# Kernel optimization log

Measured on AMD Instinct MI355X. Metric: run time of the kernel, lower is better.

## Reference

```python
import jax, jax.numpy as jnp
import numpy as np

N_FEAT = 128
F_HID = 128


def setup_inputs() -> dict:
    key = jax.random.key(0)
    ks = jax.random.split(key, 9)
    N, E = 100000, 1600000
    x = jax.random.normal(ks[0], (N, N_FEAT), dtype=jnp.float32)
    edge_index = jax.random.randint(ks[1], (2, E), 0, N, dtype=jnp.int64)
    def glorot(k, fan_in, fan_out):
        lim = np.sqrt(6.0 / (fan_in + fan_out)).astype(np.float32)
        return jax.random.uniform(k, (fan_in, fan_out), jnp.float32, -lim, lim)
    return {
        "x": x,
        "edge_index": edge_index,
        "W1": glorot(ks[2], N_FEAT, F_HID), "b1": jnp.zeros((F_HID,), jnp.float32),
        "W2": glorot(ks[3], F_HID, F_HID), "b2": jnp.zeros((F_HID,), jnp.float32),
        "W3": glorot(ks[4], F_HID, F_HID), "b3": jnp.zeros((F_HID,), jnp.float32),
    }


def _gcn_conv(x, W, b, row, col, inv_sqrt_deg, n):
    # GCNConv: x' = D^{-1/2} (A + I) D^{-1/2} (x @ W) + b  (self-loops already in row/col)
    h = x @ W                                   # [N, F]
    norm = inv_sqrt_deg[row] * inv_sqrt_deg[col]  # [E']
    msg = h[col] * norm[:, None]                # gather + scale, [E', F]
    out = jax.ops.segment_sum(msg, row, num_segments=n)  # scatter-add, [N, F]
    return out + b


def reference(x, edge_index, W1, b1, W2, b2, W3, b3):
    n = x.shape[0]
    loops = jnp.arange(n, dtype=edge_index.dtype)
    row = jnp.concatenate([edge_index[0], loops])
    col = jnp.concatenate([edge_index[1], loops])
    deg = jax.ops.segment_sum(jnp.ones_like(row, dtype=x.dtype), row, num_segments=n)
    inv_sqrt_deg = jnp.where(deg > 0, jax.lax.rsqrt(jnp.maximum(deg, 1.0)), 0.0)
    h = _gcn_conv(x, W1, b1, row, col, inv_sqrt_deg, n)
    h = jax.nn.relu(h)  # dropout is identity in eval mode
    h = _gcn_conv(h, W2, b2, row, col, inv_sqrt_deg, n)
    h = jax.nn.relu(h)
    h = _gcn_conv(h, W3, b3, row, col, inv_sqrt_deg, n)
    return h
```

## Files before the change

kernel.cpp:

```cpp
#include <hip/hip_runtime.h>
#include <hip/hip_bf16.h>

#define NFEAT 128
#define EPB   4096
#define RPB   256
#define NBU_PAD 512
#define BCAP  6144

typedef short bf16x8 __attribute__((ext_vector_type(8)));
typedef float f32x4  __attribute__((ext_vector_type(4)));

__global__ __launch_bounds__(256) void a1_hist(const int* __restrict__ rows, int E,
                                               int* __restrict__ countsT, int nbu) {
    __shared__ int h[NBU_PAD];
    int t = threadIdx.x;
    for (int i = t; i < NBU_PAD; i += 256) h[i] = 0;
    __syncthreads();
    int e0 = blockIdx.x * EPB;
    int ecnt = min(EPB, E - e0);
    for (int k = t; k < ecnt; k += 256) atomicAdd(&h[rows[e0 + k] >> 8], 1);
    __syncthreads();
    for (int j = t; j < nbu; j += 256) countsT[(size_t)blockIdx.x * nbu + j] = h[j];
}

__global__ void transpose_counts(const int* __restrict__ in, int* __restrict__ out,
                                 int nbk, int nbu) {
    int i = blockIdx.x * 256 + threadIdx.x;
    if (i < nbk * nbu) {
        int b = i / nbk, blk = i - b * nbk;
        out[i] = in[(size_t)blk * nbu + b];
    }
}

#define SCAN_B 1024
__global__ void scanA_kernel(const int* __restrict__ in, int K,
                             int* __restrict__ excl, int* __restrict__ bsums) {
    __shared__ int sm[SCAN_B];
    int t = threadIdx.x;
    int g = blockIdx.x * SCAN_B + t;
    int v = (g < K) ? in[g] : 0;
    sm[t] = v;
    __syncthreads();
    for (int off = 1; off < SCAN_B; off <<= 1) {
        int u = (t >= off) ? sm[t - off] : 0;
        __syncthreads();
        sm[t] += u;
        __syncthreads();
    }
    if (g < K) excl[g] = sm[t] - v;
    if (t == SCAN_B - 1) bsums[blockIdx.x] = sm[t];
}

__global__ void scanB_kernel(int* __restrict__ bsums, int nb) {
    __shared__ int s[256];
    int t = threadIdx.x;
    int v = (t < nb) ? bsums[t] : 0;
    s[t] = v;
    __syncthreads();
    for (int off = 1; off < 256; off <<= 1) {
        int u = (t >= off) ? s[t - off] : 0;
        __syncthreads();
        s[t] += u;
        __syncthreads();
    }
    if (t < nb) bsums[t] = s[t] - v;
}

__global__ void scanC_kernel(int* __restrict__ excl, const int* __restrict__ bsums, int K) {
    int g = blockIdx.x * 256 + threadIdx.x;
    if (g < K) excl[g] += bsums[g >> 10];
}

__global__ __launch_bounds__(256) void a2_scatter(const int* __restrict__ rows,
                                                  const int* __restrict__ colsIn, int E,
                                                  const int* __restrict__ scanArr,
                                                  int nbk, int nbu,
                                                  int* __restrict__ packed) {
    __shared__ int cnt[NBU_PAD], start[NBU_PAD], cur[NBU_PAD];
    __shared__ int sortedV[EPB];
    __shared__ unsigned short sortedB[EPB];
    __shared__ int p[256];
    int t = threadIdx.x, blk = blockIdx.x;
    for (int i = t; i < NBU_PAD; i += 256) cnt[i] = 0;
    __syncthreads();
    int e0 = blk * EPB;
    int ecnt = min(EPB, E - e0);
    int myr[16], myc[16];
#pragma unroll
    for (int k = 0; k < 16; ++k) {
        int idx = k * 256 + t;
        if (idx < ecnt) {
            myr[k] = rows[e0 + idx];
            myc[k] = colsIn[e0 + idx];
            atomicAdd(&cnt[myr[k] >> 8], 1);
        }
    }
    __syncthreads();
    int a0 = cnt[2 * t], a1 = cnt[2 * t + 1];
    p[t] = a0 + a1;
    __syncthreads();
    for (int off = 1; off < 256; off <<= 1) {
        int u = (t >= off) ? p[t - off] : 0;
        __syncthreads();
        p[t] += u;
        __syncthreads();
    }
    int ex = p[t] - (a0 + a1);
    start[2 * t] = ex;      start[2 * t + 1] = ex + a0;
    cur[2 * t] = ex;        cur[2 * t + 1] = ex + a0;
    __syncthreads();
#pragma unroll
    for (int k = 0; k < 16; ++k) {
        int idx = k * 256 + t;
        if (idx < ecnt) {
            int b = myr[k] >> 8;
            int pos = atomicAdd(&cur[b], 1);
            sortedV[pos] = ((myr[k] & 255) << 17) | myc[k];
            sortedB[pos] = (unsigned short)b;
        }
    }
    __syncthreads();
    for (int j = t; j < nbu; j += 256) cnt[j] = scanArr[(size_t)j * nbk + blk] - start[j];
    __syncthreads();
    for (int i = t; i < ecnt; i += 256) {
        int b = sortedB[i];
        packed[cnt[b] + i] = sortedV[i];
    }
}

__global__ __launch_bounds__(256) void b_sort(const int* __restrict__ packed,
                                              const int* __restrict__ scanArr,
                                              int nbk, int nbu, int N, int E,
                                              int* __restrict__ colSort,
                                              int* __restrict__ row_ptr,
                                              float* __restrict__ inv) {
    __shared__ int cnt[RPB], start[RPB], cur[RPB], s[RPB];
    __shared__ int sv[BCAP];
    int t = threadIdx.x, b = blockIdx.x;
    int base = scanArr[(size_t)b * nbk];
    int nxt = (b + 1 < nbu) ? scanArr[(size_t)(b + 1) * nbk] : E;
    int sz = nxt - base;
    cnt[t] = 0;
    __syncthreads();
    for (int i = t; i < sz; i += 256) atomicAdd(&cnt[(packed[base + i] >> 17) & 255], 1);
    __syncthreads();
    int c = cnt[t];
    s[t] = c;
    __syncthreads();
    for (int off = 1; off < 256; off <<= 1) {
        int u = (t >= off) ? s[t - off] : 0;
        __syncthreads();
        s[t] += u;
        __syncthreads();
    }
    start[t] = s[t] - c;
    cur[t] = s[t] - c;
    __syncthreads();
    for (int i = t; i < sz; i += 256) {
        int v = packed[base + i];
        int lr = (v >> 17) & 255;
        int pos = atomicAdd(&cur[lr], 1);
        if (pos < BCAP) sv[pos] = v & 0x1FFFF;
    }
    __syncthreads();
    for (int i = t; i < sz; i += 256) colSort[base + i] = sv[i];
    int r = b * RPB + t;
    if (r < N) {
        row_ptr[r] = base + start[t];
        inv[r] = rsqrtf((float)(c + 1));
    }
    if (b == 0 && t == 0) row_ptr[N] = E;
}

__device__ inline unsigned short f2bf(float x) {
    unsigned u = __float_as_uint(x);
    unsigned r = (u + 0x7FFFu + ((u >> 16) & 1u)) >> 16;
    return (unsigned short)r;
}

__device__ inline void split2(float x0, float x1, unsigned& hw, unsigned& lw) {
    unsigned u0 = __float_as_uint(x0), u1 = __float_as_uint(x1);
    hw = (u1 & 0xFFFF0000u) | (u0 >> 16);
    float l0 = x0 - __uint_as_float(u0 & 0xFFFF0000u);
    float l1 = x1 - __uint_as_float(u1 & 0xFFFF0000u);
    lw = (__float_as_uint(l1) & 0xFFFF0000u) | (__float_as_uint(l0) >> 16);
}

__global__ void wsplit_kernel(const float* __restrict__ W,
                              unsigned short* __restrict__ Wt_hi,
                              unsigned short* __restrict__ Wt_lo) {
    int i = blockIdx.x * 256 + threadIdx.x;
    int c = i >> 7, k = i & 127;
    float w = W[k * NFEAT + c];
    unsigned u = __float_as_uint(w);
    unsigned hib = u & 0xFFFF0000u;
    float lo = w - __uint_as_float(hib);
    Wt_hi[i] = (unsigned short)(u >> 16);
    Wt_lo[i] = (unsigned short)(__float_as_uint(lo) >> 16);
}

__global__ __launch_bounds__(256) void gemm_mfma(const float* __restrict__ X,
                                                 const unsigned short* __restrict__ Wt_hi,
                                                 const unsigned short* __restrict__ Wt_lo,
                                                 const float* __restrict__ inv,
                                                 unsigned short* __restrict__ Hn, int n) {
    int tid = threadIdx.x;
    int wave = tid >> 6, lane = tid & 63;
    int lrow = lane & 15, kgrp = lane >> 4;
    int wcol0 = wave * 32;
    int rowbase = blockIdx.x * 64;

    bf16x8 bh[2][4], bl[2][4];
#pragma unroll
    for (int ct = 0; ct < 2; ++ct) {
        int col = wcol0 + ct * 16 + lrow;
        const unsigned short* ph = Wt_hi + (size_t)col * NFEAT + kgrp * 8;
        const unsigned short* pl = Wt_lo + (size_t)col * NFEAT + kgrp * 8;
#pragma unroll
        for (int ks = 0; ks < 4; ++ks) {
            bh[ct][ks] = *(const bf16x8*)(ph + ks * 32);
            bl[ct][ks] = *(const bf16x8*)(pl + ks * 32);
        }
    }

    union U8 { bf16x8 v; unsigned w[4]; };

#pragma unroll
    for (int rt = 0; rt < 4; ++rt) {
        int arow = rowbase + rt * 16 + lrow;
        int rc = arow < n ? arow : n - 1;
        const float* px = X + (size_t)rc * NFEAT + kgrp * 8;

        bf16x8 ah[4], al[4];
#pragma unroll
        for (int ks = 0; ks < 4; ++ks) {
            float4 v0 = *(const float4*)(px + ks * 32);
            float4 v1 = *(const float4*)(px + ks * 32 + 4);
            U8 uh, ul;
            split2(v0.x, v0.y, uh.w[0], ul.w[0]);
            split2(v0.z, v0.w, uh.w[1], ul.w[1]);
            split2(v1.x, v1.y, uh.w[2], ul.w[2]);
            split2(v1.z, v1.w, uh.w[3], ul.w[3]);
            ah[ks] = uh.v;
            al[ks] = ul.v;
        }

        f32x4 acc[2] = {{0.f, 0.f, 0.f, 0.f}, {0.f, 0.f, 0.f, 0.f}};
#pragma unroll
        for (int ks = 0; ks < 4; ++ks) {
#pragma unroll
            for (int ct = 0; ct < 2; ++ct) {
                acc[ct] = __builtin_amdgcn_mfma_f32_16x16x32_bf16(ah[ks], bh[ct][ks], acc[ct], 0, 0, 0);
                acc[ct] = __builtin_amdgcn_mfma_f32_16x16x32_bf16(ah[ks], bl[ct][ks], acc[ct], 0, 0, 0);
                acc[ct] = __builtin_amdgcn_mfma_f32_16x16x32_bf16(al[ks], bh[ct][ks], acc[ct], 0, 0, 0);
            }
        }

#pragma unroll
        for (int m = 0; m < 4; ++m) {
            int orow = rowbase + rt * 16 + kgrp * 4 + m;
            if (orow < n) {
                float sc = inv[orow];
#pragma unroll
                for (int ct = 0; ct < 2; ++ct) {
                    int col = wcol0 + ct * 16 + lrow;
                    Hn[(size_t)orow * NFEAT + col] = f2bf(acc[ct][m] * sc);
                }
            }
        }
    }
}

template <int RELU>
__global__ __launch_bounds__(256) void aggregate_bf16(const unsigned short* __restrict__ Hn,
                                                      const int* __restrict__ row_ptr,
                                                      const int* __restrict__ cols,
                                                      const float* __restrict__ inv,
                                                      const float* __restrict__ bias,
                                                      float* __restrict__ out, int n) {
    int node = blockIdx.x * (blockDim.x >> 6) + (threadIdx.x >> 6);
    if (node >= n) return;
    int lane = threadIdx.x & 63;
    int q = lane >> 4;
    int f = (lane & 15) << 3;

    float acc[8];
#pragma unroll
    for (int k = 0; k < 8; ++k) acc[k] = 0.f;

    if (q == 0) {
        uint4 v = *(const uint4*)(Hn + (size_t)node * NFEAT + f);
        const unsigned* u = (const unsigned*)&v;
#pragma unroll
        for (int k = 0; k < 4; ++k) {
            acc[2 * k]     = __uint_as_float(u[k] << 16);
            acc[2 * k + 1] = __uint_as_float(u[k] & 0xFFFF0000u);
        }
    }

    int s = row_ptr[node], e = row_ptr[node + 1];
    for (int j = s + q; j < e; j += 4) {
        int c = cols[j];
        uint4 v = *(const uint4*)(Hn + (size_t)c * NFEAT + f);
        const unsigned* u = (const unsigned*)&v;
#pragma unroll
        for (int k = 0; k < 4; ++k) {
            acc[2 * k]     += __uint_as_float(u[k] << 16);
            acc[2 * k + 1] += __uint_as_float(u[k] & 0xFFFF0000u);
        }
    }

#pragma unroll
    for (int k = 0; k < 8; ++k) {
        acc[k] += __shfl_xor(acc[k], 16, 64);
        acc[k] += __shfl_xor(acc[k], 32, 64);
    }

    if (q == 0) {
        float inv_i = inv[node];
        float4 b0 = *(const float4*)(bias + f);
        float4 b1v = *(const float4*)(bias + f + 4);
        float r[8];
        r[0] = acc[0] * inv_i + b0.x; r[1] = acc[1] * inv_i + b0.y;
        r[2] = acc[2] * inv_i + b0.z; r[3] = acc[3] * inv_i + b0.w;
        r[4] = acc[4] * inv_i + b1v.x; r[5] = acc[5] * inv_i + b1v.y;
        r[6] = acc[6] * inv_i + b1v.z; r[7] = acc[7] * inv_i + b1v.w;
        if (RELU) {
#pragma unroll
            for (int k = 0; k < 8; ++k) r[k] = fmaxf(r[k], 0.f);
        }
        *(float4*)(out + (size_t)node * NFEAT + f)     = make_float4(r[0], r[1], r[2], r[3]);
        *(float4*)(out + (size_t)node * NFEAT + f + 4) = make_float4(r[4], r[5], r[6], r[7]);
    }
}

static inline size_t align256(size_t x) { return (x + 255) & ~(size_t)255; }

extern "C" void kernel_launch(void* const* d_in, const int* in_sizes, int n_in,
                              void* d_out, int out_size, void* d_ws, size_t ws_size,
                              hipStream_t stream) {
    const float* x   = (const float*)d_in[0];
    const int*   ei  = (const int*)d_in[1];
    const float* W1  = (const float*)d_in[2];
    const float* b1  = (const float*)d_in[3];
    const float* W2  = (const float*)d_in[4];
    const float* b2  = (const float*)d_in[5];
    const float* W3  = (const float*)d_in[6];
    const float* b3  = (const float*)d_in[7];
    float* out = (float*)d_out;

    const int N = in_sizes[0] / NFEAT;
    const int E = in_sizes[1] / 2;
    const int* rows = ei;
    const int* colsIn = ei + E;

    const int nbk = (E + EPB - 1) / EPB;
    const int nbu = (N + RPB - 1) / RPB;
    const int K = nbk * nbu;

    char* ws = (char*)d_ws;
    size_t off = 0;
    unsigned short* Hn = (unsigned short*)(ws + off);
    off = align256(off + (size_t)N * NFEAT * sizeof(unsigned short));
    int*   bufA    = (int*)(ws + off);   off = align256(off + (size_t)K * sizeof(int));
    int*   bufB    = (int*)(ws + off);   off = align256(off + (size_t)K * sizeof(int));
    int*   bsums   = (int*)(ws + off);   off = align256(off + (size_t)256 * sizeof(int));
    int*   packed  = (int*)(ws + off);   off = align256(off + (size_t)E * sizeof(int));
    int*   colSort = (int*)(ws + off);   off = align256(off + (size_t)E * sizeof(int));
    int*   row_ptr = (int*)(ws + off);   off = align256(off + (size_t)(N + 1) * sizeof(int));
    float* inv     = (float*)(ws + off); off = align256(off + (size_t)N * sizeof(float));
    unsigned short* Wt[6];
    for (int i = 0; i < 6; ++i) {
        Wt[i] = (unsigned short*)(ws + off);
        off = align256(off + (size_t)NFEAT * NFEAT * sizeof(unsigned short));
    }
    (void)ws_size; (void)n_in; (void)out_size;

    const int nb2 = (K + SCAN_B - 1) / SCAN_B;

    wsplit_kernel<<<64, 256, 0, stream>>>(W1, Wt[0], Wt[1]);
    wsplit_kernel<<<64, 256, 0, stream>>>(W2, Wt[2], Wt[3]);
    wsplit_kernel<<<64, 256, 0, stream>>>(W3, Wt[4], Wt[5]);

    a1_hist<<<nbk, 256, 0, stream>>>(rows, E, bufA, nbu);
    transpose_counts<<<(K + 255) / 256, 256, 0, stream>>>(bufA, bufB, nbk, nbu);
    scanA_kernel<<<nb2, SCAN_B, 0, stream>>>(bufB, K, bufA, bsums);
    scanB_kernel<<<1, 256, 0, stream>>>(bsums, nb2);
    scanC_kernel<<<(K + 255) / 256, 256, 0, stream>>>(bufA, bsums, K);
    a2_scatter<<<nbk, 256, 0, stream>>>(rows, colsIn, E, bufA, nbk, nbu, packed);
    b_sort<<<nbu, 256, 0, stream>>>(packed, bufA, nbk, nbu, N, E, colSort, row_ptr, inv);

    const int gemm_grid = (N + 63) / 64;
    const int agg_grid  = (N + 3) / 4;

    gemm_mfma<<<gemm_grid, 256, 0, stream>>>(x, Wt[0], Wt[1], inv, Hn, N);
    aggregate_bf16<1><<<agg_grid, 256, 0, stream>>>(Hn, row_ptr, colSort, inv, b1, out, N);
    gemm_mfma<<<gemm_grid, 256, 0, stream>>>(out, Wt[2], Wt[3], inv, Hn, N);
    aggregate_bf16<1><<<agg_grid, 256, 0, stream>>>(Hn, row_ptr, colSort, inv, b2, out, N);
    gemm_mfma<<<gemm_grid, 256, 0, stream>>>(out, Wt[4], Wt[5], inv, Hn, N);
    aggregate_bf16<0><<<agg_grid, 256, 0, stream>>>(Hn, row_ptr, colSort, inv, b3, out, N);
}
```

Measured before the change: 416.4 us.

## Emit pre-split bf16 hi/lo activations from aggregation and unroll gather loop

The hidden-layer aggregation kernels now write their output as pre-split bf16 hi/lo halves instead of fp32. A new GEMM variant consumes these halves directly, which skips the split work inside the GEMM. The total bytes written and read between layers stay the same, but the GEMM loses its conversion ALU work. The gather loop is also unrolled by two with independent accumulators to get more loads in flight, and the three weight-split launches are merged into one. The lo part is rounded to bf16 a second time, which slightly changes numerics.

After: 388.4 us. 1.07x faster.

```diff
diff --git a/kernel.cpp b/kernel.cpp
--- a/kernel.cpp
+++ b/kernel.cpp
@@ -186,24 +186,27 @@
     lw = (__float_as_uint(l1) & 0xFFFF0000u) | (__float_as_uint(l0) >> 16);
 }
 
-__global__ void wsplit_kernel(const float* __restrict__ W,
-                              unsigned short* __restrict__ Wt_hi,
-                              unsigned short* __restrict__ Wt_lo) {
+__global__ void wsplit3_kernel(const float* __restrict__ W1, const float* __restrict__ W2,
+                               const float* __restrict__ W3,
+                               unsigned short* __restrict__ WtH,
+                               unsigned short* __restrict__ WtL) {
+    int w = blockIdx.y;
+    const float* W = (w == 0) ? W1 : (w == 1) ? W2 : W3;
     int i = blockIdx.x * 256 + threadIdx.x;
     int c = i >> 7, k = i & 127;
-    float w = W[k * NFEAT + c];
-    unsigned u = __float_as_uint(w);
+    float wv = W[k * NFEAT + c];
+    unsigned u = __float_as_uint(wv);
     unsigned hib = u & 0xFFFF0000u;
-    float lo = w - __uint_as_float(hib);
-    Wt_hi[i] = (unsigned short)(u >> 16);
-    Wt_lo[i] = (unsigned short)(__float_as_uint(lo) >> 16);
-}
-
-__global__ __launch_bounds__(256) void gemm_mfma(const float* __restrict__ X,
-                                                 const unsigned short* __restrict__ Wt_hi,
-                                                 const unsigned short* __restrict__ Wt_lo,
-                                                 const float* __restrict__ inv,
-                                                 unsigned short* __restrict__ Hn, int n) {
+    float lo = wv - __uint_as_float(hib);
+    WtH[w * NFEAT * NFEAT + i] = (unsigned short)(u >> 16);
+    WtL[w * NFEAT * NFEAT + i] = (unsigned short)(__float_as_uint(lo) >> 16);
+}
+
+__global__ __launch_bounds__(256) void gemm_mfma_f32(const float* __restrict__ X,
+                                                     const unsigned short* __restrict__ Wt_hi,
+                                                     const unsigned short* __restrict__ Wt_lo,
+                                                     const float* __restrict__ inv,
+                                                     unsigned short* __restrict__ Hn, int n) {
     int tid = threadIdx.x;
     int wave = tid >> 6, lane = tid & 63;
     int lrow = lane & 15, kgrp = lane >> 4;
@@ -271,22 +274,89 @@
     }
 }
 
-template <int RELU>
+__global__ __launch_bounds__(256) void gemm_mfma_bf16(const unsigned short* __restrict__ XH,
+                                                      const unsigned short* __restrict__ XL,
+                                                      const unsigned short* __restrict__ Wt_hi,
+                                                      const unsigned short* __restrict__ Wt_lo,
+                                                      const float* __restrict__ inv,
+                                                      unsigned short* __restrict__ Hn, int n) {
+    int tid = threadIdx.x;
+    int wave = tid >> 6, lane = tid & 63;
+    int lrow = lane & 15, kgrp = lane >> 4;
+    int wcol0 = wave * 32;
+    int rowbase = blockIdx.x * 64;
+
+    bf16x8 bh[2][4], bl[2][4];
+#pragma unroll
+    for (int ct = 0; ct < 2; ++ct) {
+        int col = wcol0 + ct * 16 + lrow;
+        const unsigned short* ph = Wt_hi + (size_t)col * NFEAT + kgrp * 8;
+        const unsigned short* pl = Wt_lo + (size_t)col * NFEAT + kgrp * 8;
+#pragma unroll
+        for (int ks = 0; ks < 4; ++ks) {
+            bh[ct][ks] = *(const bf16x8*)(ph + ks * 32);
+            bl[ct][ks] = *(const bf16x8*)(pl + ks * 32);
+        }
+    }
+
+#pragma unroll
+    for (int rt = 0; rt < 4; ++rt) {
+        int arow = rowbase + rt * 16 + lrow;
+        int rc = arow < n ? arow : n - 1;
+        const unsigned short* pxh = XH + (size_t)rc * NFEAT + kgrp * 8;
+        const unsigned short* pxl = XL + (size_t)rc * NFEAT + kgrp * 8;
+
+        bf16x8 ah[4], al[4];
+#pragma unroll
+        for (int ks = 0; ks < 4; ++ks) {
+            ah[ks] = *(const bf16x8*)(pxh + ks * 32);
+            al[ks] = *(const bf16x8*)(pxl + ks * 32);
+        }
+
+        f32x4 acc[2] = {{0.f, 0.f, 0.f, 0.f}, {0.f, 0.f, 0.f, 0.f}};
+#pragma unroll
+        for (int ks = 0; ks < 4; ++ks) {
+#pragma unroll
+            for (int ct = 0; ct < 2; ++ct) {
+                acc[ct] = __builtin_amdgcn_mfma_f32_16x16x32_bf16(ah[ks], bh[ct][ks], acc[ct], 0, 0, 0);
+                acc[ct] = __builtin_amdgcn_mfma_f32_16x16x32_bf16(ah[ks], bl[ct][ks], acc[ct], 0, 0, 0);
+                acc[ct] = __builtin_amdgcn_mfma_f32_16x16x32_bf16(al[ks], bh[ct][ks], acc[ct], 0, 0, 0);
+            }
+        }
+
+#pragma unroll
+        for (int m = 0; m < 4; ++m) {
+            int orow = rowbase + rt * 16 + kgrp * 4 + m;
+            if (orow < n) {
+                float sc = inv[orow];
+#pragma unroll
+                for (int ct = 0; ct < 2; ++ct) {
+                    int col = wcol0 + ct * 16 + lrow;
+                    Hn[(size_t)orow * NFEAT + col] = f2bf(acc[ct][m] * sc);
+                }
+            }
+        }
+    }
+}
+
+template <int RELU, int EMIT_SPLIT>
 __global__ __launch_bounds__(256) void aggregate_bf16(const unsigned short* __restrict__ Hn,
                                                       const int* __restrict__ row_ptr,
                                                       const int* __restrict__ cols,
                                                       const float* __restrict__ inv,
                                                       const float* __restrict__ bias,
-                                                      float* __restrict__ out, int n) {
+                                                      float* __restrict__ out,
+                                                      unsigned short* __restrict__ XH,
+                                                      unsigned short* __restrict__ XL, int n) {
     int node = blockIdx.x * (blockDim.x >> 6) + (threadIdx.x >> 6);
     if (node >= n) return;
     int lane = threadIdx.x & 63;
     int q = lane >> 4;
     int f = (lane & 15) << 3;
 
-    float acc[8];
-#pragma unroll
-    for (int k = 0; k < 8; ++k) acc[k] = 0.f;
+    float acc[8], acc2[8];
+#pragma unroll
+    for (int k = 0; k < 8; ++k) { acc[k] = 0.f; acc2[k] = 0.f; }
 
     if (q == 0) {
         uint4 v = *(const uint4*)(Hn + (size_t)node * NFEAT + f);
@@ -299,16 +369,34 @@
     }
 
     int s = row_ptr[node], e = row_ptr[node + 1];
-    for (int j = s + q; j < e; j += 4) {
-        int c = cols[j];
-        uint4 v = *(const uint4*)(Hn + (size_t)c * NFEAT + f);
-        const unsigned* u = (const unsigned*)&v;
+    int j = s + q;
+    for (; j + 4 < e; j += 8) {
+        int ca = cols[j];
+        int cb = cols[j + 4];
+        uint4 va = *(const uint4*)(Hn + (size_t)ca * NFEAT + f);
+        uint4 vb = *(const uint4*)(Hn + (size_t)cb * NFEAT + f);
+        const unsigned* ua = (const unsigned*)&va;
+        const unsigned* ub = (const unsigned*)&vb;
 #pragma unroll
         for (int k = 0; k < 4; ++k) {
-            acc[2 * k]     += __uint_as_float(u[k] << 16);
-            acc[2 * k + 1] += __uint_as_float(u[k] & 0xFFFF0000u);
-        }
-    }
+            acc[2 * k]      += __uint_as_float(ua[k] << 16);
+            acc[2 * k + 1]  += __uint_as_float(ua[k] & 0xFFFF0000u);
+            acc2[2 * k]     += __uint_as_float(ub[k] << 16);
+            acc2[2 * k + 1] += __uint_as_float(ub[k] & 0xFFFF0000u);
+        }
+    }
+    if (j < e) {
+        int ca = cols[j];
+        uint4 va = *(const uint4*)(Hn + (size_t)ca * NFEAT + f);
+        const unsigned* ua = (const unsigned*)&va;
+#pragma unroll
+        for (int k = 0; k < 4; ++k) {
+            acc[2 * k]     += __uint_as_float(ua[k] << 16);
+            acc[2 * k + 1] += __uint_as_float(ua[k] & 0xFFFF0000u);
+        }
+    }
+#pragma unroll
+    for (int k = 0; k < 8; ++k) acc[k] += acc2[k];
 
 #pragma unroll
     for (int k = 0; k < 8; ++k) {
@@ -329,8 +417,28 @@
 #pragma unroll
             for (int k = 0; k < 8; ++k) r[k] = fmaxf(r[k], 0.f);
         }
-        *(float4*)(out + (size_t)node * NFEAT + f)     = make_float4(r[0], r[1], r[2], r[3]);
-        *(float4*)(out + (size_t)node * NFEAT + f + 4) = make_float4(r[4], r[5], r[6], r[7]);
+        if (EMIT_SPLIT) {
+            ushort4 hv[2], lv[2];
+#pragma unroll
+            for (int g = 0; g < 2; ++g) {
+#pragma unroll
+                for (int k = 0; k < 4; ++k) {
+                    float y = r[g * 4 + k];
+                    unsigned u = __float_as_uint(y);
+                    unsigned short hb = (unsigned short)(u >> 16);
+                    float lo = y - __uint_as_float(u & 0xFFFF0000u);
+                    ((unsigned short*)&hv[g])[k] = hb;
+                    ((unsigned short*)&lv[g])[k] = f2bf(lo);
+                }
+            }
+            *(ushort4*)(XH + (size_t)node * NFEAT + f)     = hv[0];
+            *(ushort4*)(XH + (size_t)node * NFEAT + f + 4) = hv[1];
+            *(ushort4*)(XL + (size_t)node * NFEAT + f)     = lv[0];
+            *(ushort4*)(XL + (size_t)node * NFEAT + f + 4) = lv[1];
+        } else {
+            *(float4*)(out + (size_t)node * NFEAT + f)     = make_float4(r[0], r[1], r[2], r[3]);
+            *(float4*)(out + (size_t)node * NFEAT + f + 4) = make_float4(r[4], r[5], r[6], r[7]);
+        }
     }
 }
 
@@ -362,6 +470,10 @@
     size_t off = 0;
     unsigned short* Hn = (unsigned short*)(ws + off);
     off = align256(off + (size_t)N * NFEAT * sizeof(unsigned short));
+    unsigned short* XH = (unsigned short*)(ws + off);
+    off = align256(off + (size_t)N * NFEAT * sizeof(unsigned short));
+    unsigned short* XL = (unsigned short*)(ws + off);
+    off = align256(off + (size_t)N * NFEAT * sizeof(unsigned short));
     int*   bufA    = (int*)(ws + off);   off = align256(off + (size_t)K * sizeof(int));
     int*   bufB    = (int*)(ws + off);   off = align256(off + (size_t)K * sizeof(int));
     int*   bsums   = (int*)(ws + off);   off = align256(off + (size_t)256 * sizeof(int));
@@ -369,18 +481,15 @@
     int*   colSort = (int*)(ws + off);   off = align256(off + (size_t)E * sizeof(int));
     int*   row_ptr = (int*)(ws + off);   off = align256(off + (size_t)(N + 1) * sizeof(int));
     float* inv     = (float*)(ws + off); off = align256(off + (size_t)N * sizeof(float));
-    unsigned short* Wt[6];
-    for (int i = 0; i < 6; ++i) {
-        Wt[i] = (unsigned short*)(ws + off);
-        off = align256(off + (size_t)NFEAT * NFEAT * sizeof(unsigned short));
-    }
+    unsigned short* WtH = (unsigned short*)(ws + off);
+    off = align256(off + (size_t)3 * NFEAT * NFEAT * sizeof(unsigned short));
+    unsigned short* WtL = (unsigned short*)(ws + off);
+    off = align256(off + (size_t)3 * NFEAT * NFEAT * sizeof(unsigned short));
     (void)ws_size; (void)n_in; (void)out_size;
 
     const int nb2 = (K + SCAN_B - 1) / SCAN_B;
 
-    wsplit_kernel<<<64, 256, 0, stream>>>(W1, Wt[0], Wt[1]);
-    wsplit_kernel<<<64, 256, 0, stream>>>(W2, Wt[2], Wt[3]);
-    wsplit_kernel<<<64, 256, 0, stream>>>(W3, Wt[4], Wt[5]);
+    wsplit3_kernel<<<dim3(64, 3), 256, 0, stream>>>(W1, W2, W3, WtH, WtL);
 
     a1_hist<<<nbk, 256, 0, stream>>>(rows, E, bufA, nbu);
     transpose_counts<<<(K + 255) / 256, 256, 0, stream>>>(bufA, bufB, nbk, nbu);
@@ -393,10 +502,15 @@
     const int gemm_grid = (N + 63) / 64;
     const int agg_grid  = (N + 3) / 4;
 
-    gemm_mfma<<<gemm_grid, 256, 0, stream>>>(x, Wt[0], Wt[1], inv, Hn, N);
-    aggregate_bf16<1><<<agg_grid, 256, 0, stream>>>(Hn, row_ptr, colSort, inv, b1, out, N);
-    gemm_mfma<<<gemm_grid, 256, 0, stream>>>(out, Wt[2], Wt[3], inv, Hn, N);
-    aggregate_bf16<1><<<agg_grid, 256, 0, stream>>>(Hn, row_ptr, colSort, inv, b2, out, N);
-    gemm_mfma<<<gemm_grid, 256, 0, stream>>>(out, Wt[4], Wt[5], inv, Hn, N);
-    aggregate_bf16<0><<<agg_grid, 256, 0, stream>>>(Hn, row_ptr, colSort, inv, b3, out, N);
-}
+    gemm_mfma_f32<<<gemm_grid, 256, 0, stream>>>(x, WtH, WtL, inv, Hn, N);
+    aggregate_bf16<1, 1><<<agg_grid, 256, 0, stream>>>(Hn, row_ptr, colSort, inv, b1,
+                                                       nullptr, XH, XL, N);
+    gemm_mfma_bf16<<<gemm_grid, 256, 0, stream>>>(XH, XL, WtH + NFEAT * NFEAT, WtL + NFEAT * NFEAT,
+                                                  inv, Hn, N);
+    aggregate_bf16<1, 1><<<agg_grid, 256, 0, stream>>>(Hn, row_ptr, colSort, inv, b2,
+                                                       nullptr, XH, XL, N);
+    gemm_mfma_bf16<<<gemm_grid, 256, 0, stream>>>(XH, XL, WtH + 2 * NFEAT * NFEAT,
+                                                  WtL + 2 * NFEAT * NFEAT, inv, Hn, N);
+    aggregate_bf16<0, 0><<<agg_grid, 256, 0, stream>>>(Hn, row_ptr, colSort, inv, b3,
+                                                       out, nullptr, nullptr, N);
+}
```
